# Kernel optimization log

Hardware: AMD Instinct MI355X
Metric: run time of the kernel (lower is better)

Reference implementation:

```python
import jax, jax.numpy as jnp
from jax import lax
import numpy as np

B, DIM, HEADS, L, K = 8, 128, 8, 4096, 3
INNER = DIM * HEADS
PAD = K // 2
EPS = 1e-5
SCALE = DIM ** -0.5


def setup_inputs() -> dict:
    key = jax.random.key(0)
    ks = jax.random.split(key, 32)

    def n(i, shape, s):
        return jax.random.normal(ks[i], shape, jnp.float32) * s

    inp = {"x": jax.random.normal(ks[0], (B, DIM, L), jnp.float32)}
    inp["ln1_g"] = jnp.ones((DIM,), jnp.float32)
    inp["ln1_b"] = jnp.zeros((DIM,), jnp.float32)
    for idx, p in enumerate(("q", "k", "v")):
        base = 1 + idx * 2
        inp[p + "_dw"] = n(base, (DIM, 1, K), 0.2)        # depthwise kernel
        inp[p + "_bn_g"] = jnp.ones((DIM,), jnp.float32)
        inp[p + "_bn_b"] = jnp.zeros((DIM,), jnp.float32)
        inp[p + "_bn_m"] = jnp.zeros((DIM,), jnp.float32)  # running mean
        inp[p + "_bn_v"] = jnp.ones((DIM,), jnp.float32)   # running var
        inp[p + "_pw"] = n(base + 1, (INNER, DIM), 0.05)   # 1x1 conv dim->inner
    inp["dwc_dw"] = n(8, (DIM,), 0.2)                      # kernel-1 depthwise = per-channel scale
    inp["dwc_bn_g"] = jnp.ones((DIM,), jnp.float32)
    inp["dwc_bn_b"] = jnp.zeros((DIM,), jnp.float32)
    inp["dwc_bn_m"] = jnp.zeros((DIM,), jnp.float32)
    inp["dwc_bn_v"] = jnp.ones((DIM,), jnp.float32)
    inp["dwc_pw"] = n(9, (DIM, DIM), 0.05)
    inp["out_w"] = n(10, (DIM, INNER), 0.05)
    inp["out_b"] = jnp.zeros((DIM,), jnp.float32)
    inp["ln2_g"] = jnp.ones((DIM,), jnp.float32)
    inp["ln2_b"] = jnp.zeros((DIM,), jnp.float32)
    inp["ff_w1"] = n(11, (4 * DIM, DIM), 0.05)
    inp["ff_b1"] = jnp.zeros((4 * DIM,), jnp.float32)
    inp["ff_w2"] = n(12, (DIM, 4 * DIM), 0.05)
    inp["ff_b2"] = jnp.zeros((DIM,), jnp.float32)
    return inp


def _layernorm(x, g, b):
    # channel-wise LN over axis=1 (unbiased=False variance)
    m = jnp.mean(x, axis=1, keepdims=True)
    v = jnp.var(x, axis=1, keepdims=True)
    return (x - m) / jnp.sqrt(v + EPS) * g[None, :, None] + b[None, :, None]


def _dw_block(x, dw, g, b, m, v, pw):
    # depthwise conv (k=K, same padding) -> eval-mode BN -> 1x1 conv
    y = lax.conv_general_dilated(x, dw, (1,), [(PAD, PAD)],
                                 feature_group_count=DIM,
                                 dimension_numbers=("NCH", "OIH", "NCH"))
    y = (y - m[None, :, None]) * (g / jnp.sqrt(v + EPS))[None, :, None] + b[None, :, None]
    return jnp.einsum("oi,bil->bol", pw, y)


def reference(x, ln1_g, ln1_b,
              q_dw, q_bn_g, q_bn_b, q_bn_m, q_bn_v, q_pw,
              k_dw, k_bn_g, k_bn_b, k_bn_m, k_bn_v, k_pw,
              v_dw, v_bn_g, v_bn_b, v_bn_m, v_bn_v, v_pw,
              dwc_dw, dwc_bn_g, dwc_bn_b, dwc_bn_m, dwc_bn_v, dwc_pw,
              out_w, out_b, ln2_g, ln2_b, ff_w1, ff_b1, ff_w2, ff_b2):
    # ---- attention block (PreNorm + residual) ----
    xn = _layernorm(x, ln1_g, ln1_b)
    q = _dw_block(xn, q_dw, q_bn_g, q_bn_b, q_bn_m, q_bn_v, q_pw)  # [B, INNER, L]
    k = _dw_block(xn, k_dw, k_bn_g, k_bn_b, k_bn_m, k_bn_v, k_pw)
    v = _dw_block(xn, v_dw, v_bn_g, v_bn_b, v_bn_m, v_bn_v, v_pw)

    def split(t):  # b (h d) x -> (b h) x d
        return t.reshape(B, HEADS, DIM, L).transpose(0, 1, 3, 2).reshape(B * HEADS, L, DIM)

    q, k, v = split(q), split(k), split(v)
    k_soft = jax.nn.softmax(k, axis=-1)                       # softmax over feature dim d
    kk = jnp.einsum("nxd,nxe->nde", q, k_soft) * SCALE        # [(bh), d, d]
    # DWConv gate on q (kernel-1 depthwise -> BN -> 1x1), channels = DIM
    g_ = q * dwc_dw[None, None, :]
    g_ = (g_ - dwc_bn_m) * (dwc_bn_g / jnp.sqrt(dwc_bn_v + EPS)) + dwc_bn_b
    g_ = jnp.einsum("od,nxd->nxo", dwc_pw, g_)
    gate = jax.nn.sigmoid(g_) * v
    out = jnp.einsum("nxd,nde->nxe", v, kk) + gate            # [(bh), L, d]
    out = out.reshape(B, HEADS, L, DIM).transpose(0, 1, 3, 2).reshape(B, INNER, L)
    attn = jnp.einsum("oi,bil->bol", out_w, out) + out_b[None, :, None]
    x = attn + x

    # ---- feed-forward block (PreNorm + residual) ----
    xn = _layernorm(x, ln2_g, ln2_b)
    h = jnp.einsum("oi,bil->bol", ff_w1, xn) + ff_b1[None, :, None]
    h = jax.nn.gelu(h, approximate=False)
    h = jnp.einsum("oi,bil->bol", ff_w2, h) + ff_b2[None, :, None]
    return h + x
```

## Files before the change

kernel.cpp:

```cpp
#include <hip/hip_runtime.h>
#include <hip/hip_bf16.h>
#include <math.h>

#define DI __device__ __forceinline__

namespace {

constexpr int L = 4096;
constexpr float EPS = 1e-5f;
constexpr float SCALEF = 0.08838834764831845f;

typedef unsigned short u16;
typedef unsigned int u32;
typedef __attribute__((ext_vector_type(8))) short bf16x8;
typedef __attribute__((ext_vector_type(4))) float f32x4;

DI float b2f(u16 h){ u32 u = ((u32)h) << 16; float f; __builtin_memcpy(&f, &u, 4); return f; }
DI u16 f2b(float f){ u32 u; __builtin_memcpy(&u, &f, 4); u32 r = u + 0x7fffu + ((u >> 16) & 1u); return (u16)(r >> 16); }
DI float sigmoidf(float x){ return 1.f / (1.f + __expf(-x)); }

DI int boff(int o, int d8){ return ((o >> 4) << 11) + (d8 << 7) + (((o & 15) ^ d8) << 3); }

DI int toff(int dhi, int nl, int x8){ return (dhi << 11) + (x8 << 7) + (((nl ^ x8 ^ dhi) & 15) << 3); }

DI void stage_a(const u16* __restrict__ g, int rs, u16* a_s, int tid){
  #pragma unroll
  for (int it = 0; it < 4; it++){
    int item = tid + 256 * it;
    int d8 = item & 15, l = item >> 4;
    *(uint4*)&a_s[l * 136 + d8 * 8] = *(const uint4*)&g[(size_t)l * rs + d8 * 8];
  }
}

__global__ __launch_bounds__(256) void ln_kernel(
    const float* __restrict__ x, const float* __restrict__ g,
    const float* __restrict__ bt, u16* __restrict__ o)
{
  const int tid = threadIdx.x;
  const int pos = blockIdx.x * 64 + (tid >> 2);
  const int part = tid & 3;
  const int b = pos >> 12, l = pos & (L - 1);
  const float* xb = x + (size_t)b * 128 * L + l;
  float vv[32];
  float s = 0.f, ss = 0.f;
  #pragma unroll
  for (int i = 0; i < 32; i++){
    float v = xb[(size_t)(part * 32 + i) * L];
    vv[i] = v; s += v; ss += v * v;
  }
  s += __shfl_xor(s, 1);  s += __shfl_xor(s, 2);
  ss += __shfl_xor(ss, 1); ss += __shfl_xor(ss, 2);
  const float m = s * (1.f / 128.f);
  const float rs = rsqrtf(ss * (1.f / 128.f) - m * m + EPS);
  #pragma unroll
  for (int c = 0; c < 4; c++){
    u16 pk[8];
    #pragma unroll
    for (int j = 0; j < 8; j++){
      int d = part * 32 + c * 8 + j;
      pk[j] = f2b((vv[c * 8 + j] - m) * rs * g[d] + bt[d]);
    }
    uint4 uu; __builtin_memcpy(&uu, pk, 16);
    *(uint4*)&o[(size_t)pos * 128 + part * 32 + c * 8] = uu;
  }
}

__global__ __launch_bounds__(256) void wpack_kernel(
    const float* __restrict__ q_pw, const float* __restrict__ k_pw,
    const float* __restrict__ v_pw, const float* __restrict__ out_w,
    const float* __restrict__ ff_w1, const float* __restrict__ ff_w2,
    const float* __restrict__ dwc_dw, const float* __restrict__ dwc_bng,
    const float* __restrict__ dwc_bnb, const float* __restrict__ dwc_bnm,
    const float* __restrict__ dwc_bnv, const float* __restrict__ dwc_pw,
    u16* __restrict__ wpk, u16* __restrict__ w2tb, float* __restrict__ c2)
{
  const int blk = blockIdx.x;
  if (blk < 320){
    int item = blk * 256 + threadIdx.x;
    int d8 = item & 15;
    int o  = (item >> 4) & 127;
    int t  = item >> 11;
    const float* src;
    if (t < 24){
      int p = t >> 3, h = t & 7;
      const float* pw = (p == 0) ? q_pw : (p == 1 ? k_pw : v_pw);
      src = pw + (size_t)(h * 128 + o) * 128 + d8 * 8;
    } else if (t < 32){
      src = out_w + (size_t)o * 1024 + (t - 24) * 128 + d8 * 8;
    } else if (t < 36){
      src = ff_w1 + (size_t)((t - 32) * 128 + o) * 128 + d8 * 8;
    } else {
      src = ff_w2 + (size_t)o * 512 + (t - 36) * 128 + d8 * 8;
    }
    u16 pk[8];
    #pragma unroll
    for (int j = 0; j < 8; j++) pk[j] = f2b(src[j]);
    uint4 uu; __builtin_memcpy(&uu, pk, 16);
    *(uint4*)&wpk[(size_t)t * 16384 + boff(o, d8)] = uu;
  } else if (blk < 328){
    int item = (blk - 320) * 256 + threadIdx.x;
    int d8 = item & 15;
    int e  = item >> 4;
    u16 pk[8];
    #pragma unroll
    for (int j = 0; j < 8; j++){
      int d = d8 * 8 + j;
      float sD = dwc_bng[d] * rsqrtf(dwc_bnv[d] + EPS);
      pk[j] = f2b(dwc_pw[(size_t)e * 128 + d] * dwc_dw[d] * sD);
    }
    uint4 uu; __builtin_memcpy(&uu, pk, 16);
    *(uint4*)&w2tb[boff(e, d8)] = uu;
  } else {
    int e = threadIdx.x;
    if (e < 128){
      float cacc = 0.f;
      for (int d = 0; d < 128; d++){
        float sD = dwc_bng[d] * rsqrtf(dwc_bnv[d] + EPS);
        cacc += dwc_pw[(size_t)e * 128 + d] * (dwc_bnb[d] - dwc_bnm[d] * sD);
      }
      c2[e] = cacc;
    }
  }
}

struct QkvArgs {
  const float* dw[3];
  const float* bng[3];
  const float* bnb[3];
  const float* bnm[3];
  const float* bnv[3];
  u16* outp[3];
};

__global__ __launch_bounds__(256, 3) void qkv_fused_kernel(
    const u16* __restrict__ xnb, const u16* __restrict__ wpk, QkvArgs args)
{
  __shared__ u16 y_s[64 * 136];
  __shared__ u16 w_s[128 * 128];
  __shared__ float4 coef[128];
  const int tid = threadIdx.x;
  const int lb = blockIdx.x;
  const int oh = blockIdx.y;
  const int bz = blockIdx.z;
  const int b  = bz / 3;
  const int p  = bz % 3;
  const int l0 = lb * 64;
  const int lane = tid & 63, wv = tid >> 6;
  const int nn = lane & 15, quad = lane >> 4;
  const int d8s = tid & 15;

  if (tid < 128){
    int d = tid;
    float sD = args.bng[p][d] * rsqrtf(args.bnv[p][d] + EPS);
    const float* dw = args.dw[p];
    coef[d] = make_float4(dw[d * 3] * sD, dw[d * 3 + 1] * sD, dw[d * 3 + 2] * sD,
                          args.bnb[p][d] - args.bnm[p][d] * sD);
  }
  __syncthreads();
  float4 cf[8];
  #pragma unroll
  for (int jj = 0; jj < 8; jj++) cf[jj] = coef[d8s * 8 + jj];
  #pragma unroll
  for (int it = 0; it < 4; it++){
    int l = (tid >> 4) + it * 16;
    int gl = l0 + l;
    const u16* rowp = xnb + ((size_t)b * L + gl) * 128 + d8s * 8;
    uint4 uc = *(const uint4*)rowp;
    uint4 um = (gl > 0)     ? *(const uint4*)(rowp - 128) : make_uint4(0, 0, 0, 0);
    uint4 up = (gl < L - 1) ? *(const uint4*)(rowp + 128) : make_uint4(0, 0, 0, 0);
    u16 em[8], ec[8], ep[8];
    __builtin_memcpy(em, &um, 16); __builtin_memcpy(ec, &uc, 16); __builtin_memcpy(ep, &up, 16);
    u16 pk[8];
    #pragma unroll
    for (int jj = 0; jj < 8; jj++)
      pk[jj] = f2b(cf[jj].x * b2f(em[jj]) + cf[jj].y * b2f(ec[jj]) + cf[jj].z * b2f(ep[jj]) + cf[jj].w);
    uint4 uu; __builtin_memcpy(&uu, pk, 16);
    *(uint4*)&y_s[l * 136 + d8s * 8] = uu;
  }
  __syncthreads();
  bf16x8 af[4];
  #pragma unroll
  for (int dc = 0; dc < 4; dc++)
    af[dc] = *(const bf16x8*)&y_s[(wv * 16 + nn) * 136 + ((dc << 2) + quad) * 8];

  for (int hh = 0; hh < 4; hh++){
    const int h = oh * 4 + hh;
    const int ph = p * 8 + h;
    if (hh) __syncthreads();
    const u16* src = wpk + ((size_t)ph << 14);
    #pragma unroll
    for (int it = 0; it < 8; it++){
      int idx = (tid + 256 * it) << 3;
      *(uint4*)&w_s[idx] = *(const uint4*)&src[idx];
    }
    __syncthreads();
    f32x4 acc[8];
    #pragma unroll
    for (int os = 0; os < 8; os++) acc[os] = (f32x4){0.f, 0.f, 0.f, 0.f};
    #pragma unroll
    for (int os = 0; os < 8; os++){
      #pragma unroll
      for (int dc = 0; dc < 4; dc++){
        int d8 = (dc << 2) + quad;
        bf16x8 bf = *(const bf16x8*)&w_s[(os << 11) + (d8 << 7) + ((nn ^ d8) << 3)];
        acc[os] = __builtin_amdgcn_mfma_f32_16x16x32_bf16(af[dc], bf, acc[os], 0, 0, 0);
      }
    }
    if (p == 1){
      #pragma unroll
      for (int r = 0; r < 4; r++){
        float m = acc[0][r];
        #pragma unroll
        for (int os = 1; os < 8; os++) m = fmaxf(m, acc[os][r]);
        m = fmaxf(m, __shfl_xor(m, 1));
        m = fmaxf(m, __shfl_xor(m, 2));
        m = fmaxf(m, __shfl_xor(m, 4));
        m = fmaxf(m, __shfl_xor(m, 8));
        float s = 0.f;
        #pragma unroll
        for (int os = 0; os < 8; os++){ acc[os][r] = __expf(acc[os][r] - m); s += acc[os][r]; }
        s += __shfl_xor(s, 1);
        s += __shfl_xor(s, 2);
        s += __shfl_xor(s, 4);
        s += __shfl_xor(s, 8);
        float inv = 1.f / s;
        #pragma unroll
        for (int os = 0; os < 8; os++) acc[os][r] *= inv;
      }
    }
    __syncthreads();
    u16* st = w_s;
    #pragma unroll
    for (int os = 0; os < 8; os++)
      #pragma unroll
      for (int r = 0; r < 4; r++)
        st[(wv * 16 + quad * 4 + r) * 136 + (os << 4) + nn] = f2b(acc[os][r]);
    __syncthreads();
    size_t gbase = ((size_t)(b * 8 + h) * L + l0) * 128;
    u16* outp = args.outp[p];
    #pragma unroll
    for (int it = 0; it < 4; it++){
      int row = (tid >> 4) + (it << 4);
      int c16 = tid & 15;
      *(uint4*)&outp[gbase + (size_t)row * 128 + (c16 << 3)] =
          *(const uint4*)&st[row * 136 + (c16 << 3)];
    }
  }
}

__global__ __launch_bounds__(256, 2) void kk_kernel(
    const u16* __restrict__ qt, const u16* __restrict__ kt,
    float* __restrict__ kkp)
{
  __shared__ u16 qT[16384];
  __shared__ u16 kT[16384];
  const int tid = threadIdx.x;
  const int sp = blockIdx.x;
  const int n  = blockIdx.y;
  const int d8 = tid & 15;
  const int x8 = tid >> 4;
  const int lane = tid & 63, wv = tid >> 6;
  const int nn = lane & 15, quad = lane >> 4;
  const int m4 = (wv >> 1) << 2;
  const int e4 = (wv & 1) << 2;
  const size_t gbase = ((size_t)n * L + sp * 1024) * 128;

  uint4 rq[8], rk[8];
  #pragma unroll
  for (int j = 0; j < 8; j++){
    size_t off = gbase + (size_t)(x8 * 8 + j) * 128 + d8 * 8;
    rq[j] = *(const uint4*)&qt[off];
    rk[j] = *(const uint4*)&kt[off];
  }

  f32x4 acc[4][4];
  #pragma unroll
  for (int mi = 0; mi < 4; mi++)
    #pragma unroll
    for (int ei = 0; ei < 4; ei++) acc[mi][ei] = (f32x4){0.f, 0.f, 0.f, 0.f};

  for (int c = 0; c < 8; c++){
    #pragma unroll
    for (int i = 0; i < 8; i++){
      u16 cq[8], ck[8];
      #pragma unroll
      for (int j = 0; j < 8; j++){
        u16 tmp[8];
        __builtin_memcpy(tmp, &rq[j], 16); cq[j] = tmp[i];
        __builtin_memcpy(tmp, &rk[j], 16); ck[j] = tmp[i];
      }
      int off = toff(d8 >> 1, ((d8 & 1) << 3) + i, x8);
      uint4 uq, uk;
      __builtin_memcpy(&uq, cq, 16); __builtin_memcpy(&uk, ck, 16);
      *(uint4*)&qT[off] = uq;
      *(uint4*)&kT[off] = uk;
    }
    __syncthreads();
    if (c < 7){
      #pragma unroll
      for (int j = 0; j < 8; j++){
        size_t off = gbase + (size_t)((c + 1) * 128 + x8 * 8 + j) * 128 + d8 * 8;
        rq[j] = *(const uint4*)&qt[off];
        rk[j] = *(const uint4*)&kt[off];
      }
    }
    #pragma unroll
    for (int ks = 0; ks < 4; ks++){
      int x8f = (ks << 2) + quad;
      bf16x8 af[4], bf[4];
      #pragma unroll
      for (int t = 0; t < 4; t++){
        af[t] = *(const bf16x8*)&qT[toff(m4 + t, nn, x8f)];
        bf[t] = *(const bf16x8*)&kT[toff(e4 + t, nn, x8f)];
      }
      #pragma unroll
      for (int mi = 0; mi < 4; mi++)
        #pragma unroll
        for (int ei = 0; ei < 4; ei++)
          acc[mi][ei] = __builtin_amdgcn_mfma_f32_16x16x32_bf16(af[mi], bf[ei], acc[mi][ei], 0, 0, 0);
    }
    __syncthreads();
  }

  float* op = kkp + ((size_t)(sp * 64 + n) << 14);
  #pragma unroll
  for (int mi = 0; mi < 4; mi++){
    #pragma unroll
    for (int r = 0; r < 4; r++){
      int d = (m4 << 4) + mi * 16 + quad * 4 + r;
      #pragma unroll
      for (int ei = 0; ei < 4; ei++)
        op[d * 128 + (e4 << 4) + ei * 16 + nn] = acc[mi][ei][r];
    }
  }
}

__global__ __launch_bounds__(256) void kkred_kernel(
    const float* __restrict__ kkp, u16* __restrict__ kkbb)
{
  int item = blockIdx.x * 256 + threadIdx.x;
  int e  = item & 127;
  int d8 = (item >> 7) & 15;
  int n  = item >> 11;
  u16 pk[8];
  #pragma unroll
  for (int j = 0; j < 8; j++){
    float s = 0.f;
    #pragma unroll
    for (int sp = 0; sp < 4; sp++)
      s += kkp[(size_t)sp * (64 * 16384) + n * 16384 + (d8 * 8 + j) * 128 + e];
    pk[j] = f2b(s * SCALEF);
  }
  uint4 uu; __builtin_memcpy(&uu, pk, 16);
  *(uint4*)&kkbb[(size_t)n * 16384 + boff(e, d8)] = uu;
}

__global__ __launch_bounds__(256, 3) void gateout_kernel(
    const u16* __restrict__ qt, const u16* __restrict__ vt,
    const u16* __restrict__ kkbb, const u16* __restrict__ w2tb,
    const float* __restrict__ c2, u16* __restrict__ outt)
{
  __shared__ u16 q_s[64 * 136];
  __shared__ u16 v_s[64 * 136];
  const int tid = threadIdx.x;
  const int lb = blockIdx.x;
  const int n  = blockIdx.y;
  const int l0 = lb * 64;
  const int lane = tid & 63, wv = tid >> 6;
  const int nn = lane & 15, quad = lane >> 4;
  const size_t base = ((size_t)n * L + l0) * 128;

  stage_a(qt + base, 128, q_s, tid);
  stage_a(vt + base, 128, v_s, tid);
  __syncthreads();

  bf16x8 af_q[4], af_v[4];
  #pragma unroll
  for (int dc = 0; dc < 4; dc++){
    af_q[dc] = *(const bf16x8*)&q_s[(wv * 16 + nn) * 136 + ((dc << 2) + quad) * 8];
    af_v[dc] = *(const bf16x8*)&v_s[(wv * 16 + nn) * 136 + ((dc << 2) + quad) * 8];
  }
  const u16* kb = kkbb + ((size_t)n << 14);
  f32x4 acc_o[8], acc_g[8];
  #pragma unroll
  for (int os = 0; os < 8; os++){ acc_o[os] = (f32x4){0,0,0,0}; acc_g[os] = (f32x4){0,0,0,0}; }
  #pragma unroll
  for (int os = 0; os < 8; os++){
    #pragma unroll
    for (int dc = 0; dc < 4; dc++){
      int d8 = (dc << 2) + quad;
      int off = (os << 11) + (d8 << 7) + ((nn ^ d8) << 3);
      bf16x8 bkk = *(const bf16x8*)&kb[off];
      bf16x8 bw  = *(const bf16x8*)&w2tb[off];
      acc_o[os] = __builtin_amdgcn_mfma_f32_16x16x32_bf16(af_v[dc], bkk, acc_o[os], 0, 0, 0);
      acc_g[os] = __builtin_amdgcn_mfma_f32_16x16x32_bf16(af_q[dc], bw,  acc_g[os], 0, 0, 0);
    }
  }
  __syncthreads();
  u16* st = q_s;
  #pragma unroll
  for (int os = 0; os < 8; os++){
    int e = (os << 4) + nn;
    float c2v = c2[e];
    #pragma unroll
    for (int r = 0; r < 4; r++){
      int xr = wv * 16 + quad * 4 + r;
      float ve = b2f(v_s[xr * 136 + e]);
      float val = acc_o[os][r] + sigmoidf(acc_g[os][r] + c2v) * ve;
      st[xr * 136 + e] = f2b(val);
    }
  }
  __syncthreads();
  #pragma unroll
  for (int it = 0; it < 4; it++){
    int row = (tid >> 4) + (it << 4);
    int c16 = tid & 15;
    *(uint4*)&outt[base + (size_t)row * 128 + (c16 << 3)] =
        *(const uint4*)&st[row * 136 + (c16 << 3)];
  }
}

__global__ __launch_bounds__(256, 3) void outw_kernel(
    const u16* __restrict__ outt, const u16* __restrict__ wpk,
    const float* __restrict__ out_b, const float* __restrict__ x,
    const float* __restrict__ g2, const float* __restrict__ bt2,
    float* __restrict__ x2, u16* __restrict__ xn2b)
{
  __shared__ u16 a_s[64 * 136];
  __shared__ float stf[128 * 68];
  const int tid = threadIdx.x;
  const int lb = blockIdx.x;
  const int b  = blockIdx.y;
  const int l0 = lb * 64;
  const int lane = tid & 63, wv = tid >> 6;
  const int nn = lane & 15, quad = lane >> 4;
  f32x4 acc[8];
  #pragma unroll
  for (int os = 0; os < 8; os++) acc[os] = (f32x4){0,0,0,0};

  for (int h = 0; h < 8; h++){
    __syncthreads();
    stage_a(outt + ((size_t)(b * 8 + h) * L + l0) * 128, 128, a_s, tid);
    __syncthreads();
    bf16x8 af[4];
    #pragma unroll
    for (int dc = 0; dc < 4; dc++)
      af[dc] = *(const bf16x8*)&a_s[(wv * 16 + nn) * 136 + ((dc << 2) + quad) * 8];
    const u16* bp = wpk + (size_t)(24 + h) * 16384;
    #pragma unroll
    for (int os = 0; os < 8; os++){
      #pragma unroll
      for (int dc = 0; dc < 4; dc++){
        int d8 = (dc << 2) + quad;
        bf16x8 bf = *(const bf16x8*)&bp[(os << 11) + (d8 << 7) + ((nn ^ d8) << 3)];
        acc[os] = __builtin_amdgcn_mfma_f32_16x16x32_bf16(af[dc], bf, acc[os], 0, 0, 0);
      }
    }
  }
  #pragma unroll
  for (int os = 0; os < 8; os++)
    #pragma unroll
    for (int r = 0; r < 4; r++)
      stf[((os << 4) + nn) * 68 + wv * 16 + quad * 4 + r] = acc[os][r];
  __syncthreads();
  {
    int o = tid >> 1, lh = tid & 1;
    float bias = out_b[o];
    size_t gbase = ((size_t)b * 128 + o) * L + l0 + lh * 32;
    float* sp = &stf[o * 68 + lh * 32];
    #pragma unroll
    for (int k = 0; k < 8; k++){
      float4 xv = *(const float4*)&x[gbase + k * 4];
      float4 sv = *(float4*)&sp[k * 4];
      float4 ov = make_float4(sv.x + bias + xv.x, sv.y + bias + xv.y,
                              sv.z + bias + xv.z, sv.w + bias + xv.w);
      *(float4*)&sp[k * 4] = ov;
      *(float4*)&x2[gbase + k * 4] = ov;
    }
  }
  __syncthreads();
  {
    int l = tid >> 2, part = tid & 3;
    float vv[32];
    float s = 0.f, ss = 0.f;
    #pragma unroll
    for (int i = 0; i < 32; i++){
      float v = stf[(part * 32 + i) * 68 + l];
      vv[i] = v; s += v; ss += v * v;
    }
    s += __shfl_xor(s, 1);  s += __shfl_xor(s, 2);
    ss += __shfl_xor(ss, 1); ss += __shfl_xor(ss, 2);
    float m = s * (1.f / 128.f);
    float rs = rsqrtf(ss * (1.f / 128.f) - m * m + EPS);
    #pragma unroll
    for (int c = 0; c < 4; c++){
      u16 pk[8];
      #pragma unroll
      for (int j = 0; j < 8; j++){
        int d = part * 32 + c * 8 + j;
        pk[j] = f2b((vv[c * 8 + j] - m) * rs * g2[d] + bt2[d]);
      }
      uint4 uu; __builtin_memcpy(&uu, pk, 16);
      *(uint4*)&xn2b[((size_t)b * L + l0 + l) * 128 + part * 32 + c * 8] = uu;
    }
  }
}

__global__ __launch_bounds__(256, 2) void ff_fused_kernel(
    const u16* __restrict__ xn2b, const u16* __restrict__ wpk,
    const float* __restrict__ b1, const float* __restrict__ b2,
    const float* __restrict__ x2, float* __restrict__ outp)
{
  __shared__ u16 a_s[64 * 136];
  __shared__ u16 h_s[64 * 136];
  const int tid = threadIdx.x;
  const int lb = blockIdx.x;
  const int b  = blockIdx.y;
  const int l0 = lb * 64;
  const int lane = tid & 63, wv = tid >> 6;
  const int nn = lane & 15, quad = lane >> 4;

  stage_a(xn2b + ((size_t)b * L + l0) * 128, 128, a_s, tid);
  __syncthreads();
  bf16x8 af[4];
  #pragma unroll
  for (int dc = 0; dc < 4; dc++)
    af[dc] = *(const bf16x8*)&a_s[(wv * 16 + nn) * 136 + ((dc << 2) + quad) * 8];

  f32x4 acc_out[8];
  #pragma unroll
  for (int os = 0; os < 8; os++) acc_out[os] = (f32x4){0.f, 0.f, 0.f, 0.f};

  for (int fc = 0; fc < 4; fc++){
    const u16* bp1 = wpk + (size_t)(32 + fc) * 16384;
    f32x4 hacc[8];
    #pragma unroll
    for (int os = 0; os < 8; os++) hacc[os] = (f32x4){0.f, 0.f, 0.f, 0.f};
    #pragma unroll
    for (int os = 0; os < 8; os++){
      #pragma unroll
      for (int dc = 0; dc < 4; dc++){
        int d8 = (dc << 2) + quad;
        bf16x8 bf = *(const bf16x8*)&bp1[(os << 11) + (d8 << 7) + ((nn ^ d8) << 3)];
        hacc[os] = __builtin_amdgcn_mfma_f32_16x16x32_bf16(af[dc], bf, hacc[os], 0, 0, 0);
      }
    }
    __syncthreads();
    #pragma unroll
    for (int os = 0; os < 8; os++){
      float bias = b1[fc * 128 + (os << 4) + nn];
      #pragma unroll
      for (int r = 0; r < 4; r++){
        float v = hacc[os][r] + bias;
        float ge = 0.5f * v * (1.f + erff(v * 0.70710678118654752f));
        h_s[(wv * 16 + quad * 4 + r) * 136 + (os << 4) + nn] = f2b(ge);
      }
    }
    __syncthreads();
    bf16x8 hf[4];
    #pragma unroll
    for (int dc = 0; dc < 4; dc++)
      hf[dc] = *(const bf16x8*)&h_s[(wv * 16 + nn) * 136 + ((dc << 2) + quad) * 8];
    const u16* bp2 = wpk + (size_t)(36 + fc) * 16384;
    #pragma unroll
    for (int os = 0; os < 8; os++){
      #pragma unroll
      for (int dc = 0; dc < 4; dc++){
        int d8 = (dc << 2) + quad;
        bf16x8 bf = *(const bf16x8*)&bp2[(os << 11) + (d8 << 7) + ((nn ^ d8) << 3)];
        acc_out[os] = __builtin_amdgcn_mfma_f32_16x16x32_bf16(hf[dc], bf, acc_out[os], 0, 0, 0);
      }
    }
  }

  float* stf = (float*)h_s;
  #pragma unroll
  for (int t = 0; t < 2; t++){
    __syncthreads();
    #pragma unroll
    for (int osl = 0; osl < 4; osl++){
      int os = t * 4 + osl;
      #pragma unroll
      for (int r = 0; r < 4; r++)
        stf[((osl << 4) + nn) * 68 + wv * 16 + quad * 4 + r] = acc_out[os][r];
    }
    __syncthreads();
    int ol = tid >> 2;
    int o  = t * 64 + ol;
    int lc = (tid & 3) * 16;
    float bias = b2[o];
    size_t gbase = ((size_t)b * 128 + o) * L + l0 + lc;
    #pragma unroll
    for (int k = 0; k < 4; k++){
      float4 sv = *(const float4*)&stf[ol * 68 + lc + k * 4];
      float4 xv = *(const float4*)&x2[gbase + k * 4];
      *(float4*)&outp[gbase + k * 4] = make_float4(sv.x + bias + xv.x, sv.y + bias + xv.y,
                                                   sv.z + bias + xv.z, sv.w + bias + xv.w);
    }
  }
}

}

extern "C" void kernel_launch(void* const* d_in, const int* in_sizes, int n_in,
                              void* d_out, int out_size, void* d_ws, size_t ws_size,
                              hipStream_t stream)
{
  const float* x      = (const float*)d_in[0];
  const float* ln1_g  = (const float*)d_in[1];
  const float* ln1_b  = (const float*)d_in[2];
  const float* q_dw   = (const float*)d_in[3];
  const float* q_bng  = (const float*)d_in[4];
  const float* q_bnb  = (const float*)d_in[5];
  const float* q_bnm  = (const float*)d_in[6];
  const float* q_bnv  = (const float*)d_in[7];
  const float* q_pw   = (const float*)d_in[8];
  const float* k_dw   = (const float*)d_in[9];
  const float* k_bng  = (const float*)d_in[10];
  const float* k_bnb  = (const float*)d_in[11];
  const float* k_bnm  = (const float*)d_in[12];
  const float* k_bnv  = (const float*)d_in[13];
  const float* k_pw   = (const float*)d_in[14];
  const float* v_dw   = (const float*)d_in[15];
  const float* v_bng  = (const float*)d_in[16];
  const float* v_bnb  = (const float*)d_in[17];
  const float* v_bnm  = (const float*)d_in[18];
  const float* v_bnv  = (const float*)d_in[19];
  const float* v_pw   = (const float*)d_in[20];
  const float* dwc_dw  = (const float*)d_in[21];
  const float* dwc_bng = (const float*)d_in[22];
  const float* dwc_bnb = (const float*)d_in[23];
  const float* dwc_bnm = (const float*)d_in[24];
  const float* dwc_bnv = (const float*)d_in[25];
  const float* dwc_pw  = (const float*)d_in[26];
  const float* out_w  = (const float*)d_in[27];
  const float* out_b  = (const float*)d_in[28];
  const float* ln2_g  = (const float*)d_in[29];
  const float* ln2_b  = (const float*)d_in[30];
  const float* ff_w1  = (const float*)d_in[31];
  const float* ff_b1  = (const float*)d_in[32];
  const float* ff_w2  = (const float*)d_in[33];
  const float* ff_b2  = (const float*)d_in[34];
  float* out = (float*)d_out;

  char* w = (char*)d_ws;
  u16*  qt   = (u16*)(w);
  u16*  kt   = (u16*)(w + (64ull  << 20));
  u16*  outt = kt;
  u16*  vt   = (u16*)(w + (128ull << 20));
  u16*  xnb  = (u16*)(w + (192ull << 20));
  u16*  kkbb = xnb;
  u16*  xn2b = xnb;
  float* kkp = (float*)(w + (200ull << 20));
  float* x2  = kkp;
  u16*  w2tb = (u16*)(w + (216ull << 20));
  float* c2  = (float*)(w + (216ull << 20) + 32768);
  u16*  wpk  = (u16*)(w + (216ull << 20) + 65536);

  ln_kernel<<<512, 256, 0, stream>>>(x, ln1_g, ln1_b, xnb);
  wpack_kernel<<<329, 256, 0, stream>>>(q_pw, k_pw, v_pw, out_w, ff_w1, ff_w2,
                                        dwc_dw, dwc_bng, dwc_bnb, dwc_bnm, dwc_bnv, dwc_pw,
                                        wpk, w2tb, c2);

  QkvArgs qa;
  qa.dw[0] = q_dw;  qa.bng[0] = q_bng; qa.bnb[0] = q_bnb; qa.bnm[0] = q_bnm; qa.bnv[0] = q_bnv; qa.outp[0] = qt;
  qa.dw[1] = k_dw;  qa.bng[1] = k_bng; qa.bnb[1] = k_bnb; qa.bnm[1] = k_bnm; qa.bnv[1] = k_bnv; qa.outp[1] = kt;
  qa.dw[2] = v_dw;  qa.bng[2] = v_bng; qa.bnb[2] = v_bnb; qa.bnm[2] = v_bnm; qa.bnv[2] = v_bnv; qa.outp[2] = vt;
  qkv_fused_kernel<<<dim3(64, 2, 24), 256, 0, stream>>>(xnb, wpk, qa);

  kk_kernel<<<dim3(4, 64), 256, 0, stream>>>(qt, kt, kkp);
  kkred_kernel<<<512, 256, 0, stream>>>(kkp, kkbb);
  gateout_kernel<<<dim3(64, 64), 256, 0, stream>>>(qt, vt, kkbb, w2tb, c2, outt);
  outw_kernel<<<dim3(64, 8), 256, 0, stream>>>(outt, wpk, out_b, x, ln2_g, ln2_b, x2, xn2b);

  ff_fused_kernel<<<dim3(64, 8), 256, 0, stream>>>(xn2b, wpk, ff_b1, ff_b2, x2, out);
}
```

Before: 412.1 us.

## Store v, kk, attention output and out_w in FP8 with MFMA fp8 tiles

Converts the v tensor, the reduced kk matrix, the gated attention output and the out projection weight to FP8 (with power-of-two scaling) stored in an MFMA-fragment tiled layout. The v@kk and out_w matmuls switch to fp8 MFMA instructions, and outw loads its A fragments straight from global memory without LDS staging. The aim is to roughly halve intermediate memory traffic and LDS use, allowing higher occupancy. The cost is reduced numerical precision, which may hurt accuracy tolerance.

```diff
diff --git a/kernel.cpp b/kernel.cpp
--- a/kernel.cpp
+++ b/kernel.cpp
@@ -12,6 +12,7 @@
 
 typedef unsigned short u16;
 typedef unsigned int u32;
+typedef unsigned char u8;
 typedef __attribute__((ext_vector_type(8))) short bf16x8;
 typedef __attribute__((ext_vector_type(4))) float f32x4;
 
@@ -19,9 +20,20 @@
 DI u16 f2b(float f){ u32 u; __builtin_memcpy(&u, &f, 4); u32 r = u + 0x7fffu + ((u >> 16) & 1u); return (u16)(r >> 16); }
 DI float sigmoidf(float x){ return 1.f / (1.f + __expf(-x)); }
 
+DI uint2 pack_fp8x8(const float* v){
+  u32 lo = __builtin_amdgcn_cvt_pk_fp8_f32(v[0], v[1], 0, false);
+  lo = (u32)__builtin_amdgcn_cvt_pk_fp8_f32(v[2], v[3], lo, true);
+  u32 hi = __builtin_amdgcn_cvt_pk_fp8_f32(v[4], v[5], 0, false);
+  hi = (u32)__builtin_amdgcn_cvt_pk_fp8_f32(v[6], v[7], hi, true);
+  return make_uint2(lo, hi);
+}
+DI u8 f2e(float v){ return (u8)__builtin_amdgcn_cvt_pk_fp8_f32(v, v, 0, false); }
+DI float e2f(u8 c){ return __builtin_amdgcn_cvt_f32_fp8((int)c, 0); }
+
 DI int boff(int o, int d8){ return ((o >> 4) << 11) + (d8 << 7) + (((o & 15) ^ d8) << 3); }
-
 DI int toff(int dhi, int nl, int x8){ return (dhi << 11) + (x8 << 7) + (((nl ^ x8 ^ dhi) & 15) << 3); }
+DI int foff(int g, int k8, int nn){ return (g << 11) + (k8 << 7) + (nn << 3); }
+DI int faddr(int x, int e){ return ((x >> 4) << 11) + ((e >> 3) << 7) + ((x & 15) << 3) + (e & 7); }
 
 DI void stage_a(const u16* __restrict__ g, int rs, u16* a_s, int tid){
   #pragma unroll
@@ -72,7 +84,8 @@
     const float* __restrict__ dwc_dw, const float* __restrict__ dwc_bng,
     const float* __restrict__ dwc_bnb, const float* __restrict__ dwc_bnm,
     const float* __restrict__ dwc_bnv, const float* __restrict__ dwc_pw,
-    u16* __restrict__ wpk, u16* __restrict__ w2tb, float* __restrict__ c2)
+    u16* __restrict__ wpk, u16* __restrict__ w2tb, float* __restrict__ c2,
+    u8* __restrict__ wpk8)
 {
   const int blk = blockIdx.x;
   if (blk < 320){
@@ -110,7 +123,7 @@
     }
     uint4 uu; __builtin_memcpy(&uu, pk, 16);
     *(uint4*)&w2tb[boff(e, d8)] = uu;
-  } else {
+  } else if (blk == 328){
     int e = threadIdx.x;
     if (e < 128){
       float cacc = 0.f;
@@ -120,6 +133,19 @@
       }
       c2[e] = cacc;
     }
+  } else {
+    int h = blk - 329;
+    #pragma unroll
+    for (int it = 0; it < 8; it++){
+      int item = threadIdx.x + 256 * it;
+      int nn = item & 15, k8 = (item >> 4) & 15, os = item >> 8;
+      int o = os * 16 + nn;
+      float fv[8];
+      #pragma unroll
+      for (int j = 0; j < 8; j++)
+        fv[j] = out_w[(size_t)o * 1024 + h * 128 + k8 * 8 + j] * 16.f;
+      *(uint2*)&wpk8[(h << 14) + foff(os, k8, nn)] = pack_fp8x8(fv);
+    }
   }
 }
 
@@ -129,7 +155,7 @@
   const float* bnb[3];
   const float* bnm[3];
   const float* bnv[3];
-  u16* outp[3];
+  void* outp[3];
 };
 
 __global__ __launch_bounds__(256, 3) void qkv_fused_kernel(
@@ -236,14 +262,28 @@
       for (int r = 0; r < 4; r++)
         st[(wv * 16 + quad * 4 + r) * 136 + (os << 4) + nn] = f2b(acc[os][r]);
     __syncthreads();
-    size_t gbase = ((size_t)(b * 8 + h) * L + l0) * 128;
-    u16* outp = args.outp[p];
-    #pragma unroll
-    for (int it = 0; it < 4; it++){
-      int row = (tid >> 4) + (it << 4);
-      int c16 = tid & 15;
-      *(uint4*)&outp[gbase + (size_t)row * 128 + (c16 << 3)] =
-          *(const uint4*)&st[row * 136 + (c16 << 3)];
+    if (p == 2){
+      u8* v8 = (u8*)args.outp[2];
+      size_t tbase = ((size_t)((b * 8 + h) * 64 + lb)) << 13;
+      #pragma unroll
+      for (int it = 0; it < 4; it++){
+        int g = it, e8 = tid >> 4, n2 = tid & 15;
+        const u16* sp = &st[(g * 16 + n2) * 136 + e8 * 8];
+        float fv[8];
+        #pragma unroll
+        for (int j = 0; j < 8; j++) fv[j] = b2f(sp[j]);
+        *(uint2*)&v8[tbase + foff(g, e8, n2)] = pack_fp8x8(fv);
+      }
+    } else {
+      u16* outp = (u16*)args.outp[p];
+      size_t gbase = ((size_t)(b * 8 + h) * L + l0) * 128;
+      #pragma unroll
+      for (int it = 0; it < 4; it++){
+        int row = (tid >> 4) + (it << 4);
+        int c16 = tid & 15;
+        *(uint4*)&outp[gbase + (size_t)row * 128 + (c16 << 3)] =
+            *(const uint4*)&st[row * 136 + (c16 << 3)];
+      }
     }
   }
 }
@@ -336,51 +376,54 @@
 }
 
 __global__ __launch_bounds__(256) void kkred_kernel(
-    const float* __restrict__ kkp, u16* __restrict__ kkbb)
+    const float* __restrict__ kkp, u8* __restrict__ kkbb8)
 {
   int item = blockIdx.x * 256 + threadIdx.x;
-  int e  = item & 127;
-  int d8 = (item >> 7) & 15;
-  int n  = item >> 11;
-  u16 pk[8];
+  int nn = item & 15, d8 = (item >> 4) & 15, os = (item >> 8) & 7, n = item >> 11;
+  int e = os * 16 + nn;
+  float fv[8];
   #pragma unroll
   for (int j = 0; j < 8; j++){
     float s = 0.f;
     #pragma unroll
     for (int sp = 0; sp < 4; sp++)
       s += kkp[(size_t)sp * (64 * 16384) + n * 16384 + (d8 * 8 + j) * 128 + e];
-    pk[j] = f2b(s * SCALEF);
-  }
-  uint4 uu; __builtin_memcpy(&uu, pk, 16);
-  *(uint4*)&kkbb[(size_t)n * 16384 + boff(e, d8)] = uu;
-}
-
-__global__ __launch_bounds__(256, 3) void gateout_kernel(
-    const u16* __restrict__ qt, const u16* __restrict__ vt,
-    const u16* __restrict__ kkbb, const u16* __restrict__ w2tb,
-    const float* __restrict__ c2, u16* __restrict__ outt)
+    fv[j] = s * (SCALEF * 32.f);
+  }
+  *(uint2*)&kkbb8[((size_t)n << 14) + foff(os, d8, nn)] = pack_fp8x8(fv);
+}
+
+__global__ __launch_bounds__(256, 4) void gateout_kernel(
+    const u16* __restrict__ qt, const u8* __restrict__ vt8,
+    const u8* __restrict__ kkbb8, const u16* __restrict__ w2tb,
+    const float* __restrict__ c2, u8* __restrict__ outt8)
 {
   __shared__ u16 q_s[64 * 136];
-  __shared__ u16 v_s[64 * 136];
+  __shared__ __attribute__((aligned(16))) u8 v_s8[8192];
   const int tid = threadIdx.x;
   const int lb = blockIdx.x;
   const int n  = blockIdx.y;
   const int l0 = lb * 64;
   const int lane = tid & 63, wv = tid >> 6;
   const int nn = lane & 15, quad = lane >> 4;
-  const size_t base = ((size_t)n * L + l0) * 128;
-
-  stage_a(qt + base, 128, q_s, tid);
-  stage_a(vt + base, 128, v_s, tid);
+  const size_t vtile = ((size_t)(n * 64 + lb)) << 13;
+
+  stage_a(qt + ((size_t)n * L + l0) * 128, 128, q_s, tid);
+  #pragma unroll
+  for (int it = 0; it < 2; it++){
+    int idx = (tid + 256 * it) << 4;
+    *(uint4*)&v_s8[idx] = *(const uint4*)&vt8[vtile + idx];
+  }
   __syncthreads();
 
-  bf16x8 af_q[4], af_v[4];
+  bf16x8 af_q[4];
+  long av[4];
   #pragma unroll
   for (int dc = 0; dc < 4; dc++){
     af_q[dc] = *(const bf16x8*)&q_s[(wv * 16 + nn) * 136 + ((dc << 2) + quad) * 8];
-    af_v[dc] = *(const bf16x8*)&v_s[(wv * 16 + nn) * 136 + ((dc << 2) + quad) * 8];
-  }
-  const u16* kb = kkbb + ((size_t)n << 14);
+    av[dc] = *(const long*)&v_s8[foff(wv, (dc << 2) + quad, nn)];
+  }
+  const u8* kb8 = kkbb8 + ((size_t)n << 14);
   f32x4 acc_o[8], acc_g[8];
   #pragma unroll
   for (int os = 0; os < 8; os++){ acc_o[os] = (f32x4){0,0,0,0}; acc_g[os] = (f32x4){0,0,0,0}; }
@@ -389,15 +432,14 @@
     #pragma unroll
     for (int dc = 0; dc < 4; dc++){
       int d8 = (dc << 2) + quad;
-      int off = (os << 11) + (d8 << 7) + ((nn ^ d8) << 3);
-      bf16x8 bkk = *(const bf16x8*)&kb[off];
-      bf16x8 bw  = *(const bf16x8*)&w2tb[off];
-      acc_o[os] = __builtin_amdgcn_mfma_f32_16x16x32_bf16(af_v[dc], bkk, acc_o[os], 0, 0, 0);
-      acc_g[os] = __builtin_amdgcn_mfma_f32_16x16x32_bf16(af_q[dc], bw,  acc_g[os], 0, 0, 0);
+      long bkk = *(const long*)&kb8[foff(os, d8, nn)];
+      bf16x8 bw  = *(const bf16x8*)&w2tb[(os << 11) + (d8 << 7) + ((nn ^ d8) << 3)];
+      acc_o[os] = __builtin_amdgcn_mfma_f32_16x16x32_fp8_fp8(av[dc], bkk, acc_o[os], 0, 0, 0);
+      acc_g[os] = __builtin_amdgcn_mfma_f32_16x16x32_bf16(af_q[dc], bw, acc_g[os], 0, 0, 0);
     }
   }
   __syncthreads();
-  u16* st = q_s;
+  u8* st8 = (u8*)q_s;
   #pragma unroll
   for (int os = 0; os < 8; os++){
     int e = (os << 4) + nn;
@@ -405,28 +447,25 @@
     #pragma unroll
     for (int r = 0; r < 4; r++){
       int xr = wv * 16 + quad * 4 + r;
-      float ve = b2f(v_s[xr * 136 + e]);
-      float val = acc_o[os][r] + sigmoidf(acc_g[os][r] + c2v) * ve;
-      st[xr * 136 + e] = f2b(val);
+      float ve = e2f(v_s8[faddr(xr, e)]);
+      float val = acc_o[os][r] * (1.f / 32.f) + sigmoidf(acc_g[os][r] + c2v) * ve;
+      st8[faddr(xr, e)] = f2e(val);
     }
   }
   __syncthreads();
   #pragma unroll
-  for (int it = 0; it < 4; it++){
-    int row = (tid >> 4) + (it << 4);
-    int c16 = tid & 15;
-    *(uint4*)&outt[base + (size_t)row * 128 + (c16 << 3)] =
-        *(const uint4*)&st[row * 136 + (c16 << 3)];
-  }
-}
-
-__global__ __launch_bounds__(256, 3) void outw_kernel(
-    const u16* __restrict__ outt, const u16* __restrict__ wpk,
+  for (int it = 0; it < 2; it++){
+    int idx = (tid + 256 * it) << 4;
+    *(uint4*)&outt8[vtile + idx] = *(const uint4*)&st8[idx];
+  }
+}
+
+__global__ __launch_bounds__(256, 4) void outw_kernel(
+    const u8* __restrict__ outt8, const u8* __restrict__ wpk8,
     const float* __restrict__ out_b, const float* __restrict__ x,
     const float* __restrict__ g2, const float* __restrict__ bt2,
     float* __restrict__ x2, u16* __restrict__ xn2b)
 {
-  __shared__ u16 a_s[64 * 136];
   __shared__ float stf[128 * 68];
   const int tid = threadIdx.x;
   const int lb = blockIdx.x;
@@ -439,21 +478,18 @@
   for (int os = 0; os < 8; os++) acc[os] = (f32x4){0,0,0,0};
 
   for (int h = 0; h < 8; h++){
-    __syncthreads();
-    stage_a(outt + ((size_t)(b * 8 + h) * L + l0) * 128, 128, a_s, tid);
-    __syncthreads();
-    bf16x8 af[4];
+    const size_t tbase = ((size_t)((b * 8 + h) * 64 + lb)) << 13;
+    long af[4];
     #pragma unroll
     for (int dc = 0; dc < 4; dc++)
-      af[dc] = *(const bf16x8*)&a_s[(wv * 16 + nn) * 136 + ((dc << 2) + quad) * 8];
-    const u16* bp = wpk + (size_t)(24 + h) * 16384;
+      af[dc] = *(const long*)&outt8[tbase + foff(wv, (dc << 2) + quad, nn)];
+    const u8* bp8 = wpk8 + (h << 14);
     #pragma unroll
     for (int os = 0; os < 8; os++){
       #pragma unroll
       for (int dc = 0; dc < 4; dc++){
-        int d8 = (dc << 2) + quad;
-        bf16x8 bf = *(const bf16x8*)&bp[(os << 11) + (d8 << 7) + ((nn ^ d8) << 3)];
-        acc[os] = __builtin_amdgcn_mfma_f32_16x16x32_bf16(af[dc], bf, acc[os], 0, 0, 0);
+        long bf8 = *(const long*)&bp8[foff(os, (dc << 2) + quad, nn)];
+        acc[os] = __builtin_amdgcn_mfma_f32_16x16x32_fp8_fp8(af[dc], bf8, acc[os], 0, 0, 0);
       }
     }
   }
@@ -461,7 +497,7 @@
   for (int os = 0; os < 8; os++)
     #pragma unroll
     for (int r = 0; r < 4; r++)
-      stf[((os << 4) + nn) * 68 + wv * 16 + quad * 4 + r] = acc[os][r];
+      stf[((os << 4) + nn) * 68 + wv * 16 + quad * 4 + r] = acc[os][r] * 0.0625f;
   __syncthreads();
   {
     int o = tid >> 1, lh = tid & 1;
@@ -644,34 +680,35 @@
   float* out = (float*)d_out;
 
   char* w = (char*)d_ws;
-  u16*  qt   = (u16*)(w);
-  u16*  kt   = (u16*)(w + (64ull  << 20));
-  u16*  outt = kt;
-  u16*  vt   = (u16*)(w + (128ull << 20));
-  u16*  xnb  = (u16*)(w + (192ull << 20));
-  u16*  kkbb = xnb;
-  u16*  xn2b = xnb;
-  float* kkp = (float*)(w + (200ull << 20));
-  float* x2  = kkp;
-  u16*  w2tb = (u16*)(w + (216ull << 20));
-  float* c2  = (float*)(w + (216ull << 20) + 32768);
-  u16*  wpk  = (u16*)(w + (216ull << 20) + 65536);
+  u16*  qt    = (u16*)(w);
+  u16*  kt    = (u16*)(w + (64ull  << 20));
+  u8*   outt8 = (u8*)(w + (64ull  << 20));
+  u8*   vt8   = (u8*)(w + (128ull << 20));
+  u16*  xnb   = (u16*)(w + (192ull << 20));
+  u8*   kkbb8 = (u8*)(w + (192ull << 20));
+  u16*  xn2b  = (u16*)(w + (192ull << 20));
+  float* kkp  = (float*)(w + (200ull << 20));
+  float* x2   = kkp;
+  u16*  w2tb  = (u16*)(w + (216ull << 20));
+  float* c2   = (float*)(w + (216ull << 20) + 32768);
+  u16*  wpk   = (u16*)(w + (216ull << 20) + 65536);
+  u8*   wpk8  = (u8*)(w + (218ull << 20));
 
   ln_kernel<<<512, 256, 0, stream>>>(x, ln1_g, ln1_b, xnb);
-  wpack_kernel<<<329, 256, 0, stream>>>(q_pw, k_pw, v_pw, out_w, ff_w1, ff_w2,
+  wpack_kernel<<<337, 256, 0, stream>>>(q_pw, k_pw, v_pw, out_w, ff_w1, ff_w2,
                                         dwc_dw, dwc_bng, dwc_bnb, dwc_bnm, dwc_bnv, dwc_pw,
-                                        wpk, w2tb, c2);
+                                        wpk, w2tb, c2, wpk8);
 
   QkvArgs qa;
   qa.dw[0] = q_dw;  qa.bng[0] = q_bng; qa.bnb[0] = q_bnb; qa.bnm[0] = q_bnm; qa.bnv[0] = q_bnv; qa.outp[0] = qt;
   qa.dw[1] = k_dw;  qa.bng[1] = k_bng; qa.bnb[1] = k_bnb; qa.bnm[1] = k_bnm; qa.bnv[1] = k_bnv; qa.outp[1] = kt;
-  qa.dw[2] = v_dw;  qa.bng[2] = v_bng; qa.bnb[2] = v_bnb; qa.bnm[2] = v_bnm; qa.bnv[2] = v_bnv; qa.outp[2] = vt;
+  qa.dw[2] = v_dw;  qa.bng[2] = v_bng; qa.bnb[2] = v_bnb; qa.bnm[2] = v_bnm; qa.bnv[2] = v_bnv; qa.outp[2] = vt8;
   qkv_fused_kernel<<<dim3(64, 2, 24), 256, 0, stream>>>(xnb, wpk, qa);
 
   kk_kernel<<<dim3(4, 64), 256, 0, stream>>>(qt, kt, kkp);
-  kkred_kernel<<<512, 256, 0, stream>>>(kkp, kkbb);
-  gateout_kernel<<<dim3(64, 64), 256, 0, stream>>>(qt, vt, kkbb, w2tb, c2, outt);
-  outw_kernel<<<dim3(64, 8), 256, 0, stream>>>(outt, wpk, out_b, x, ln2_g, ln2_b, x2, xn2b);
+  kkred_kernel<<<512, 256, 0, stream>>>(kkp, kkbb8);
+  gateout_kernel<<<dim3(64, 64), 256, 0, stream>>>(qt, vt8, kkbb8, w2tb, c2, outt8);
+  outw_kernel<<<dim3(64, 8), 256, 0, stream>>>(outt8, wpk8, out_b, x, ln2_g, ln2_b, x2, xn2b);
 
   ff_fused_kernel<<<dim3(64, 8), 256, 0, stream>>>(xn2b, wpk, ff_b1, ff_b2, x2, out);
 }
```

After: 378.3 us. 8.2% less time.
